# Optimization experiments

Hardware: AMD Instinct MI355X
Metric: run time of the kernel (lower is better)

The kernel has to match this reference:

```python
import jax, jax.numpy as jnp
import numpy as np

IN_DIM = 256
OUT_DIM = 256


def setup_inputs() -> dict:
    key = jax.random.key(0)
    k1, k2, k3, k4 = jax.random.split(key, 4)
    B, N = 8, 2048
    X = jax.random.normal(k1, (B, N, IN_DIM), dtype=jnp.float32)
    adj = jax.random.uniform(k2, (B, N, N), dtype=jnp.float32)
    # nn.Linear(input_dim, output_dim): W is [out, in], bias [out]
    bound = 1.0 / np.sqrt(IN_DIM)
    W = jax.random.uniform(k3, (OUT_DIM, IN_DIM), minval=-bound, maxval=bound, dtype=jnp.float32)
    b = jax.random.uniform(k4, (OUT_DIM,), minval=-bound, maxval=bound, dtype=jnp.float32)
    return {"X": X, "adj": adj, "W": W, "b": b}


def reference(X, adj, W, b):
    N = adj.shape[-1]
    # adj_hat = adj + I
    adj_hat = adj + jnp.eye(N, dtype=adj.dtype)
    # D^{-1/2} A_hat D^{-1/2}: diag matmuls are just row/col scaling
    d = jnp.sum(adj_hat, axis=-1) ** -0.5  # [B, N]
    adj_norm = d[..., :, None] * adj_hat * d[..., None, :]
    # aggregate then linear + relu
    H = jnp.matmul(adj_norm, X)  # [B, N, F_in]
    out = jnp.einsum('bnf,of->bno', H, W) + b
    return jax.nn.relu(out)
```

## Files before the change

kernel.cpp:

```cpp
#include <hip/hip_runtime.h>
#include <stdint.h>

typedef __attribute__((ext_vector_type(8))) short bf16x8;
typedef __attribute__((ext_vector_type(4))) float f32x4;
typedef unsigned short u16;

constexpr int NN = 2048, NF = 256;

__device__ inline u16 f2bf(float f) {
  uint32_t u = __builtin_bit_cast(uint32_t, f);
  uint32_t r = (u + 0x7FFFu + ((u >> 16) & 1u)) >> 16;
  return (u16)r;
}
__device__ inline float bf2f(u16 h) {
  uint32_t u = ((uint32_t)h) << 16;
  return __builtin_bit_cast(float, u);
}

__device__ inline void gload_lds16(const void* g, void* l) {
  __builtin_amdgcn_global_load_lds(
      (const __attribute__((address_space(1))) uint32_t*)g,
      (__attribute__((address_space(3))) uint32_t*)l,
      16, 0, 0);
}

__global__ __launch_bounds__(256) void k_rowsum(const float* __restrict__ adj,
                                                u16* __restrict__ adjb,
                                                float* __restrict__ d,
                                                const float* __restrict__ W,
                                                u16* __restrict__ Wb) {
  if (blockIdx.x >= 16384) {
    int i = (blockIdx.x - 16384) * 256 + threadIdx.x;
    float4 v = ((const float4*)W)[i];
    ushort4 o;
    o.x = f2bf(v.x); o.y = f2bf(v.y); o.z = f2bf(v.z); o.w = f2bf(v.w);
    *(ushort4*)(Wb + (size_t)i * 4) = o;
    return;
  }
  int row = blockIdx.x;
  const float4* p = (const float4*)(adj + (size_t)row * NN);
  u16* ob = adjb + (size_t)row * NN;
  float s = 0.f;
#pragma unroll
  for (int c = 0; c < 2; ++c) {
    int idx = threadIdx.x + 256 * c;
    float4 v = p[idx];
    s += v.x + v.y + v.z + v.w;
    ushort4 o;
    o.x = f2bf(v.x); o.y = f2bf(v.y); o.z = f2bf(v.z); o.w = f2bf(v.w);
    *(ushort4*)(ob + (size_t)idx * 4) = o;
  }
#pragma unroll
  for (int off = 32; off > 0; off >>= 1) s += __shfl_down(s, off, 64);
  __shared__ float red[4];
  int lane = threadIdx.x & 63, w = threadIdx.x >> 6;
  if (lane == 0) red[w] = s;
  __syncthreads();
  if (threadIdx.x == 0) {
    float t = red[0] + red[1] + red[2] + red[3] + 1.0f;
    d[row] = 1.0f / sqrtf(t);
  }
}

__global__ __launch_bounds__(256) void k_xprep(const float* __restrict__ X,
                                               const float* __restrict__ d,
                                               u16* __restrict__ XpT) {
  int jt = blockIdx.x, ft = blockIdx.y, b = blockIdx.z;
  int j0 = jt * 64, f0 = ft * 64;
  __shared__ u16 T[64][66];
  int t = threadIdx.x;
#pragma unroll
  for (int s = 0; s < 4; ++s) {
    int q = s * 256 + t;
    int r = q >> 4, c4 = q & 15;
    int j = j0 + r;
    float dv = d[b * NN + j];
    float4 v = *(const float4*)(X + ((size_t)(b * NN + j)) * NF + f0 + c4 * 4);
    T[r][c4 * 4 + 0] = f2bf(v.x * dv);
    T[r][c4 * 4 + 1] = f2bf(v.y * dv);
    T[r][c4 * 4 + 2] = f2bf(v.z * dv);
    T[r][c4 * 4 + 3] = f2bf(v.w * dv);
  }
  __syncthreads();
#pragma unroll
  for (int s = 0; s < 4; ++s) {
    int q = s * 256 + t;
    int fr = q >> 4, c4 = q & 15;
    int f = f0 + fr;
    int swz = (f >> 1) & 3;
    int joff = (c4 * 4) ^ (swz << 3);
    ushort4 o;
    o.x = T[c4 * 4 + 0][fr]; o.y = T[c4 * 4 + 1][fr];
    o.z = T[c4 * 4 + 2][fr]; o.w = T[c4 * 4 + 3][fr];
    *(ushort4*)(XpT + ((size_t)(b * NF + f)) * NN + j0 + joff) = o;
  }
}

#define BBASE 12288

#define FUSED_STEP(K, AW, AR, BW, BRI, VMC, IA, IB)                            \
  {                                                                            \
    if (IA) {                                                                  \
      gload_lds16(a_src + (size_t)((K) + 2) * 32,                              \
                  smem + ((AW) << 12) + (w << 10));                            \
    }                                                                          \
    if (IB) {                                                                  \
      _Pragma("unroll")                                                        \
      for (int c = 0; c < 4; ++c) {                                            \
        int q = c * 256 + t;                                                   \
        gload_lds16(XpTb + (size_t)(q >> 2) * NN + ((K) + 2) * 32 + (q & 3) * 8, \
                    smem + BBASE + ((BW) << 14) + (c * 256 + w * 64) * 16);    \
      }                                                                        \
    }                                                                          \
    __builtin_amdgcn_sched_barrier(0);                                         \
    asm volatile("s_waitcnt vmcnt(" VMC ")" ::: "memory");                     \
    __builtin_amdgcn_sched_barrier(0);                                         \
    __builtin_amdgcn_s_barrier();                                              \
    __builtin_amdgcn_sched_barrier(0);                                         \
    const char* Ab = smem + ((AR) << 12) + (((K) & 1) << 11);                  \
    const char* Bb = smem + BBASE + ((BRI) << 14);                             \
    bf16x8 af0 = *(const bf16x8*)(Ab + aoff0);                                 \
    bf16x8 af1 = *(const bf16x8*)(Ab + aoff0 + 1024);                          \
    bf16x8 b0 = *(const bf16x8*)(Bb + boff0);                                  \
    bf16x8 b1 = *(const bf16x8*)(Bb + boff0 + 1024);                           \
    bf16x8 b2 = *(const bf16x8*)(Bb + boff0 + 2048);                           \
    bf16x8 b3 = *(const bf16x8*)(Bb + boff0 + 3072);                           \
    asm volatile("s_waitcnt lgkmcnt(0)" ::: "memory");                         \
    __builtin_amdgcn_sched_barrier(0);                                         \
    __builtin_amdgcn_s_setprio(1);                                             \
    acc[0][0] = __builtin_amdgcn_mfma_f32_16x16x32_bf16(af0, b0, acc[0][0], 0, 0, 0); \
    acc[0][1] = __builtin_amdgcn_mfma_f32_16x16x32_bf16(af0, b1, acc[0][1], 0, 0, 0); \
    acc[0][2] = __builtin_amdgcn_mfma_f32_16x16x32_bf16(af0, b2, acc[0][2], 0, 0, 0); \
    acc[0][3] = __builtin_amdgcn_mfma_f32_16x16x32_bf16(af0, b3, acc[0][3], 0, 0, 0); \
    acc[1][0] = __builtin_amdgcn_mfma_f32_16x16x32_bf16(af1, b0, acc[1][0], 0, 0, 0); \
    acc[1][1] = __builtin_amdgcn_mfma_f32_16x16x32_bf16(af1, b1, acc[1][1], 0, 0, 0); \
    acc[1][2] = __builtin_amdgcn_mfma_f32_16x16x32_bf16(af1, b2, acc[1][2], 0, 0, 0); \
    acc[1][3] = __builtin_amdgcn_mfma_f32_16x16x32_bf16(af1, b3, acc[1][3], 0, 0, 0); \
    __builtin_amdgcn_s_setprio(0);                                             \
    __builtin_amdgcn_sched_barrier(0);                                         \
  }

__global__ __launch_bounds__(256, 2) void k_fused(
    const u16* __restrict__ adjb, const u16* __restrict__ XpT,
    const float* __restrict__ dsc, const u16* __restrict__ Wb,
    const float* __restrict__ bias, float* __restrict__ out) {
  int flat = blockIdx.x;
  int b = flat & 7, mt = flat >> 3;
  int i0 = mt * 32;

  __shared__ __align__(16) char smem[77824];
  u16* Hs = (u16*)smem;

  int t = threadIdx.x;
  int lane = t & 63, w = t >> 6;
  int l15 = lane & 15, l4 = lane >> 4;
  int wc = w;

  const u16* adjbb = adjb + ((size_t)b * NN + i0) * NN;
  const u16* XpTb = XpT + (size_t)b * NF * NN;

  int as_ = t >> 7, ar_ = (t >> 2) & 31, ac_ = t & 3;
  const u16* a_src = adjbb + (size_t)ar_ * NN + as_ * 32 +
                     ((ac_ ^ ((ar_ >> 1) & 3)) << 3);

  int aoff0 = l15 * 64 + ((l4 ^ ((l15 >> 1) & 3)) << 4);
  int n0 = wc * 64 + l15;
  int boff0 = n0 * 64 + ((l4 ^ ((n0 >> 1) & 3)) << 4);

  f32x4 acc[2][4] = {};

  gload_lds16(a_src, smem + (w << 10));
#pragma unroll
  for (int c = 0; c < 4; ++c) {
    int q = c * 256 + t;
    gload_lds16(XpTb + (size_t)(q >> 2) * NN + (q & 3) * 8,
                smem + BBASE + (c * 256 + w * 64) * 16);
  }
#pragma unroll
  for (int c = 0; c < 4; ++c) {
    int q = c * 256 + t;
    gload_lds16(XpTb + (size_t)(q >> 2) * NN + 32 + (q & 3) * 8,
                smem + BBASE + 16384 + (c * 256 + w * 64) * 16);
  }
  __builtin_amdgcn_sched_barrier(0);

  for (int kb = 0; kb < 60; kb += 12) {
    FUSED_STEP(kb + 0, 1, 0, 2, 0, "9", 1, 1)
    FUSED_STEP(kb + 1, 0, 0, 3, 1, "9", 0, 1)
    FUSED_STEP(kb + 2, 2, 1, 0, 2, "9", 1, 1)
    FUSED_STEP(kb + 3, 0, 1, 1, 3, "9", 0, 1)
    FUSED_STEP(kb + 4, 0, 2, 2, 0, "9", 1, 1)
    FUSED_STEP(kb + 5, 0, 2, 3, 1, "9", 0, 1)
    FUSED_STEP(kb + 6, 1, 0, 0, 2, "9", 1, 1)
    FUSED_STEP(kb + 7, 0, 0, 1, 3, "9", 0, 1)
    FUSED_STEP(kb + 8, 2, 1, 2, 0, "9", 1, 1)
    FUSED_STEP(kb + 9, 0, 1, 3, 1, "9", 0, 1)
    FUSED_STEP(kb + 10, 0, 2, 0, 2, "9", 1, 1)
    FUSED_STEP(kb + 11, 0, 2, 1, 3, "9", 0, 1)
  }
  FUSED_STEP(60, 1, 0, 2, 0, "9", 1, 1)
  FUSED_STEP(61, 0, 0, 3, 1, "9", 0, 1)
  FUSED_STEP(62, 0, 1, 0, 2, "4", 0, 0)
  FUSED_STEP(63, 0, 1, 0, 3, "0", 0, 0)

  __syncthreads();

  const float* db = dsc + b * NN;
#pragma unroll
  for (int mi = 0; mi < 2; ++mi) {
#pragma unroll
    for (int ni = 0; ni < 4; ++ni) {
      int f = wc * 64 + ni * 16 + l15;
      int swz8 = ((f >> 1) & 3) << 3;
      ushort4 xv = *(const ushort4*)(XpTb + (size_t)f * NN + i0 +
                                     ((mi * 16 + l4 * 4) ^ swz8));
#pragma unroll
      for (int qq = 0; qq < 4; ++qq) {
        int il = mi * 16 + l4 * 4 + qq;
        float dv = db[i0 + il];
        float xpv = bf2f(((const u16*)&xv)[qq]);
        float hv = dv * (acc[mi][ni][qq] + xpv);
        Hs[il * 264 + f] = f2bf(hv);
      }
    }
  }
  __syncthreads();

  f32x4 acc2[2][4] = {};
#pragma unroll
  for (int kk = 0; kk < 256; kk += 32) {
    bf16x8 a2[2], b2[4];
#pragma unroll
    for (int mi = 0; mi < 2; ++mi) {
      int r = mi * 16 + l15;
      a2[mi] = *(const bf16x8*)&Hs[r * 264 + kk + l4 * 8];
    }
#pragma unroll
    for (int ni = 0; ni < 4; ++ni) {
      int o = wc * 64 + ni * 16 + l15;
      b2[ni] = *(const bf16x8*)&Wb[(size_t)o * 256 + kk + l4 * 8];
    }
#pragma unroll
    for (int mi = 0; mi < 2; ++mi)
#pragma unroll
      for (int ni = 0; ni < 4; ++ni)
        acc2[mi][ni] = __builtin_amdgcn_mfma_f32_16x16x32_bf16(a2[mi], b2[ni],
                                                               acc2[mi][ni], 0, 0, 0);
  }

  float* outb = out + ((size_t)b * NN + i0) * NF;
#pragma unroll
  for (int mi = 0; mi < 2; ++mi) {
#pragma unroll
    for (int qq = 0; qq < 4; ++qq) {
      int il = mi * 16 + l4 * 4 + qq;
#pragma unroll
      for (int ni = 0; ni < 4; ++ni) {
        int o = wc * 64 + ni * 16 + l15;
        float v = acc2[mi][ni][qq] + bias[o];
        outb[(size_t)il * NF + o] = fmaxf(v, 0.f);
      }
    }
  }
}

extern "C" void kernel_launch(void* const* d_in, const int* in_sizes, int n_in,
                              void* d_out, int out_size, void* d_ws, size_t ws_size,
                              hipStream_t stream) {
  const float* X    = (const float*)d_in[0];
  const float* adj  = (const float*)d_in[1];
  const float* W    = (const float*)d_in[2];
  const float* bias = (const float*)d_in[3];
  float* out = (float*)d_out;

  char* ws = (char*)d_ws;
  float* dsc  = (float*)(ws);
  u16*   Wb   = (u16*)(ws + 65536);
  u16*   XpT  = (u16*)(ws + 262144);
  u16*   adjb = (u16*)(ws + 262144 + 8388608);

  k_rowsum<<<dim3(16448), dim3(256), 0, stream>>>(adj, adjb, dsc, W, Wb);
  k_xprep<<<dim3(32, 4, 8), dim3(256), 0, stream>>>(X, dsc, XpT);
  k_fused<<<dim3(512), dim3(256), 0, stream>>>(adjb, XpT, dsc, Wb, bias, out);
}
```

Measured before the change: 85.12 us.

## Double fused-kernel row tile to 64 with 8 waves sharing XpT tiles

The fused kernel now processes 64 output rows per block with 512 threads (2x4 wave grid) instead of 32 rows with 256 threads. Each XpT tile staged in LDS is reused by twice as many rows, which halves global/L2 traffic for the dense operand. The XOR swizzle moves from the stored XpT layout to the load addresses. The pipeline buffer indices and vmcnt waits are retuned for the new load counts. Cost: only 256 blocks (fewer than before) and more LDS per block, which may reduce occupancy and load balance across CUs.

New measurement: 75.68 us. -11.1%, faster.

```diff
diff --git a/kernel.cpp b/kernel.cpp
--- a/kernel.cpp
+++ b/kernel.cpp
@@ -86,39 +86,32 @@
   for (int s = 0; s < 4; ++s) {
     int q = s * 256 + t;
     int fr = q >> 4, c4 = q & 15;
-    int f = f0 + fr;
-    int swz = (f >> 1) & 3;
-    int joff = (c4 * 4) ^ (swz << 3);
     ushort4 o;
     o.x = T[c4 * 4 + 0][fr]; o.y = T[c4 * 4 + 1][fr];
     o.z = T[c4 * 4 + 2][fr]; o.w = T[c4 * 4 + 3][fr];
-    *(ushort4*)(XpT + ((size_t)(b * NF + f)) * NN + j0 + joff) = o;
-  }
-}
-
-#define BBASE 12288
-
-#define FUSED_STEP(K, AW, AR, BW, BRI, VMC, IA, IB)                            \
+    *(ushort4*)(XpT + ((size_t)(b * NF + f0 + fr)) * NN + j0 + c4 * 4) = o;
+  }
+}
+
+#define BBASE 24576
+
+#define FUSED_STEP(K, ARB, H, AW, BW, VMC, IA, IB)                             \
   {                                                                            \
-    if (IA) {                                                                  \
-      gload_lds16(a_src + (size_t)((K) + 2) * 32,                              \
-                  smem + ((AW) << 12) + (w << 10));                            \
+    if (IA) gload_lds16(a_src + (size_t)((K) + 2) * 32,                        \
+                        smem + (AW) * 8192 + aw_dst);                          \
+    if (IB) {                                                                  \
+      gload_lds16(b_src0 + (size_t)((K) + 2) * 32,                            \
+                  smem + BBASE + (BW) * 16384 + bw_dst0);                      \
+      gload_lds16(b_src1 + (size_t)((K) + 2) * 32,                            \
+                  smem + BBASE + (BW) * 16384 + bw_dst1);                      \
     }                                                                          \
-    if (IB) {                                                                  \
-      _Pragma("unroll")                                                        \
-      for (int c = 0; c < 4; ++c) {                                            \
-        int q = c * 256 + t;                                                   \
-        gload_lds16(XpTb + (size_t)(q >> 2) * NN + ((K) + 2) * 32 + (q & 3) * 8, \
-                    smem + BBASE + ((BW) << 14) + (c * 256 + w * 64) * 16);    \
-      }                                                                        \
-    }                                                                          \
     __builtin_amdgcn_sched_barrier(0);                                         \
     asm volatile("s_waitcnt vmcnt(" VMC ")" ::: "memory");                     \
     __builtin_amdgcn_sched_barrier(0);                                         \
     __builtin_amdgcn_s_barrier();                                              \
     __builtin_amdgcn_sched_barrier(0);                                         \
-    const char* Ab = smem + ((AR) << 12) + (((K) & 1) << 11);                  \
-    const char* Bb = smem + BBASE + ((BRI) << 14);                             \
+    const char* Ab = smem + (ARB) * 8192 + ((H) << 12);                        \
+    const char* Bb = smem + BBASE + ((K) & 3) * 16384;                         \
     bf16x8 af0 = *(const bf16x8*)(Ab + aoff0);                                 \
     bf16x8 af1 = *(const bf16x8*)(Ab + aoff0 + 1024);                          \
     bf16x8 b0 = *(const bf16x8*)(Bb + boff0);                                  \
@@ -140,68 +133,72 @@
     __builtin_amdgcn_sched_barrier(0);                                         \
   }
 
-__global__ __launch_bounds__(256, 2) void k_fused(
+__global__ __launch_bounds__(512, 2) void k_fused(
     const u16* __restrict__ adjb, const u16* __restrict__ XpT,
     const float* __restrict__ dsc, const u16* __restrict__ Wb,
     const float* __restrict__ bias, float* __restrict__ out) {
   int flat = blockIdx.x;
   int b = flat & 7, mt = flat >> 3;
-  int i0 = mt * 32;
-
-  __shared__ __align__(16) char smem[77824];
+  int i0 = mt * 64;
+
+  __shared__ __align__(16) char smem[90112];
   u16* Hs = (u16*)smem;
 
   int t = threadIdx.x;
   int lane = t & 63, w = t >> 6;
   int l15 = lane & 15, l4 = lane >> 4;
-  int wc = w;
+  int wr = w >> 2, wc = w & 3;
 
   const u16* adjbb = adjb + ((size_t)b * NN + i0) * NN;
   const u16* XpTb = XpT + (size_t)b * NF * NN;
 
-  int as_ = t >> 7, ar_ = (t >> 2) & 31, ac_ = t & 3;
-  const u16* a_src = adjbb + (size_t)ar_ * NN + as_ * 32 +
-                     ((ac_ ^ ((ar_ >> 1) & 3)) << 3);
-
-  int aoff0 = l15 * 64 + ((l4 ^ ((l15 >> 1) & 3)) << 4);
-  int n0 = wc * 64 + l15;
-  int boff0 = n0 * 64 + ((l4 ^ ((n0 >> 1) & 3)) << 4);
+  int sA = (w << 6) + lane;
+  int uA = sA >> 8;
+  int rA = (sA >> 2) & 63;
+  int cA = sA & 3;
+  const u16* a_src = adjbb + (size_t)rA * NN + uA * 32 +
+                     ((cA ^ ((rA >> 1) & 3)) << 3);
+  int aw_dst = w << 10;
+
+  int n0s = sA >> 2, c0s = sA & 3;
+  const u16* b_src0 = XpTb + (size_t)n0s * NN + ((c0s ^ ((n0s >> 1) & 3)) << 3);
+  int s1 = 512 + sA;
+  int n1s = s1 >> 2, c1s = s1 & 3;
+  const u16* b_src1 = XpTb + (size_t)n1s * NN + ((c1s ^ ((n1s >> 1) & 3)) << 3);
+  int bw_dst0 = w << 10;
+  int bw_dst1 = 8192 + (w << 10);
+
+  int swz = (l4 ^ ((l15 >> 1) & 3)) << 4;
+  int aoff0 = (wr * 32 + l15) * 64 + swz;
+  int boff0 = (wc * 64 + l15) * 64 + swz;
 
   f32x4 acc[2][4] = {};
 
-  gload_lds16(a_src, smem + (w << 10));
-#pragma unroll
-  for (int c = 0; c < 4; ++c) {
-    int q = c * 256 + t;
-    gload_lds16(XpTb + (size_t)(q >> 2) * NN + (q & 3) * 8,
-                smem + BBASE + (c * 256 + w * 64) * 16);
-  }
-#pragma unroll
-  for (int c = 0; c < 4; ++c) {
-    int q = c * 256 + t;
-    gload_lds16(XpTb + (size_t)(q >> 2) * NN + 32 + (q & 3) * 8,
-                smem + BBASE + 16384 + (c * 256 + w * 64) * 16);
-  }
+  gload_lds16(a_src, smem + aw_dst);
+  gload_lds16(b_src0, smem + BBASE + bw_dst0);
+  gload_lds16(b_src1, smem + BBASE + bw_dst1);
+  gload_lds16(b_src0 + 32, smem + BBASE + 16384 + bw_dst0);
+  gload_lds16(b_src1 + 32, smem + BBASE + 16384 + bw_dst1);
   __builtin_amdgcn_sched_barrier(0);
 
   for (int kb = 0; kb < 60; kb += 12) {
-    FUSED_STEP(kb + 0, 1, 0, 2, 0, "9", 1, 1)
-    FUSED_STEP(kb + 1, 0, 0, 3, 1, "9", 0, 1)
-    FUSED_STEP(kb + 2, 2, 1, 0, 2, "9", 1, 1)
-    FUSED_STEP(kb + 3, 0, 1, 1, 3, "9", 0, 1)
-    FUSED_STEP(kb + 4, 0, 2, 2, 0, "9", 1, 1)
-    FUSED_STEP(kb + 5, 0, 2, 3, 1, "9", 0, 1)
-    FUSED_STEP(kb + 6, 1, 0, 0, 2, "9", 1, 1)
-    FUSED_STEP(kb + 7, 0, 0, 1, 3, "9", 0, 1)
-    FUSED_STEP(kb + 8, 2, 1, 2, 0, "9", 1, 1)
-    FUSED_STEP(kb + 9, 0, 1, 3, 1, "9", 0, 1)
-    FUSED_STEP(kb + 10, 0, 2, 0, 2, "9", 1, 1)
-    FUSED_STEP(kb + 11, 0, 2, 1, 3, "9", 0, 1)
-  }
-  FUSED_STEP(60, 1, 0, 2, 0, "9", 1, 1)
-  FUSED_STEP(61, 0, 0, 3, 1, "9", 0, 1)
-  FUSED_STEP(62, 0, 1, 0, 2, "4", 0, 0)
-  FUSED_STEP(63, 0, 1, 0, 3, "0", 0, 0)
+    FUSED_STEP(kb + 0, 0, 0, 1, 2, "5", 1, 1)
+    FUSED_STEP(kb + 1, 0, 1, 0, 3, "5", 0, 1)
+    FUSED_STEP(kb + 2, 1, 0, 2, 0, "5", 1, 1)
+    FUSED_STEP(kb + 3, 1, 1, 0, 1, "5", 0, 1)
+    FUSED_STEP(kb + 4, 2, 0, 0, 2, "5", 1, 1)
+    FUSED_STEP(kb + 5, 2, 1, 0, 3, "5", 0, 1)
+    FUSED_STEP(kb + 6, 0, 0, 1, 0, "5", 1, 1)
+    FUSED_STEP(kb + 7, 0, 1, 0, 1, "5", 0, 1)
+    FUSED_STEP(kb + 8, 1, 0, 2, 2, "5", 1, 1)
+    FUSED_STEP(kb + 9, 1, 1, 0, 3, "5", 0, 1)
+    FUSED_STEP(kb + 10, 2, 0, 0, 0, "5", 1, 1)
+    FUSED_STEP(kb + 11, 2, 1, 0, 1, "5", 0, 1)
+  }
+  FUSED_STEP(60, 0, 0, 1, 2, "5", 1, 1)
+  FUSED_STEP(61, 0, 1, 0, 3, "5", 0, 1)
+  FUSED_STEP(62, 1, 0, 0, 0, "2", 0, 0)
+  FUSED_STEP(63, 1, 1, 0, 0, "0", 0, 0)
 
   __syncthreads();
 
@@ -211,12 +208,11 @@
 #pragma unroll
     for (int ni = 0; ni < 4; ++ni) {
       int f = wc * 64 + ni * 16 + l15;
-      int swz8 = ((f >> 1) & 3) << 3;
       ushort4 xv = *(const ushort4*)(XpTb + (size_t)f * NN + i0 +
-                                     ((mi * 16 + l4 * 4) ^ swz8));
+                                     wr * 32 + mi * 16 + l4 * 4);
 #pragma unroll
       for (int qq = 0; qq < 4; ++qq) {
-        int il = mi * 16 + l4 * 4 + qq;
+        int il = wr * 32 + mi * 16 + l4 * 4 + qq;
         float dv = db[i0 + il];
         float xpv = bf2f(((const u16*)&xv)[qq]);
         float hv = dv * (acc[mi][ni][qq] + xpv);
@@ -232,7 +228,7 @@
     bf16x8 a2[2], b2[4];
 #pragma unroll
     for (int mi = 0; mi < 2; ++mi) {
-      int r = mi * 16 + l15;
+      int r = wr * 32 + mi * 16 + l15;
       a2[mi] = *(const bf16x8*)&Hs[r * 264 + kk + l4 * 8];
     }
 #pragma unroll
@@ -253,7 +249,7 @@
   for (int mi = 0; mi < 2; ++mi) {
 #pragma unroll
     for (int qq = 0; qq < 4; ++qq) {
-      int il = mi * 16 + l4 * 4 + qq;
+      int il = wr * 32 + mi * 16 + l4 * 4 + qq;
 #pragma unroll
       for (int ni = 0; ni < 4; ++ni) {
         int o = wc * 64 + ni * 16 + l15;
@@ -281,5 +277,5 @@
 
   k_rowsum<<<dim3(16448), dim3(256), 0, stream>>>(adj, adjb, dsc, W, Wb);
   k_xprep<<<dim3(32, 4, 8), dim3(256), 0, stream>>>(X, dsc, XpT);
-  k_fused<<<dim3(512), dim3(256), 0, stream>>>(adjb, XpT, dsc, Wb, bias, out);
-}
+  k_fused<<<dim3(256), dim3(512), 0, stream>>>(adjb, XpT, dsc, Wb, bias, out);
+}
```

## Drop bf16 adjacency copy; convert fp32 adj to bf16 inside fused GEMM

Applied to the files above, without the earlier changes.

The rowsum kernel no longer writes a bf16 copy of the adjacency matrix. The fused kernel now loads fp32 adj tiles into registers three steps ahead, converts them to bf16 and stores them into a triple-buffered swizzled LDS area. The swizzle for X moves from the prep kernel's global layout to the fused kernel's load addressing, and the MFMA sequence is split around a partial lgkmcnt wait. This removes a 64MB bf16 write and read of adj, but the fused kernel must read 128MB of fp32 adj and spend VGPRs and ALU work on conversion inside the main loop.

Result: faster. 82.52 us (-3.1%).

```diff
diff --git a/kernel.cpp b/kernel.cpp
--- a/kernel.cpp
+++ b/kernel.cpp
@@ -25,7 +25,6 @@
 }
 
 __global__ __launch_bounds__(256) void k_rowsum(const float* __restrict__ adj,
-                                                u16* __restrict__ adjb,
                                                 float* __restrict__ d,
                                                 const float* __restrict__ W,
                                                 u16* __restrict__ Wb) {
@@ -39,16 +38,11 @@
   }
   int row = blockIdx.x;
   const float4* p = (const float4*)(adj + (size_t)row * NN);
-  u16* ob = adjb + (size_t)row * NN;
   float s = 0.f;
 #pragma unroll
   for (int c = 0; c < 2; ++c) {
-    int idx = threadIdx.x + 256 * c;
-    float4 v = p[idx];
+    float4 v = p[threadIdx.x + 256 * c];
     s += v.x + v.y + v.z + v.w;
-    ushort4 o;
-    o.x = f2bf(v.x); o.y = f2bf(v.y); o.z = f2bf(v.z); o.w = f2bf(v.w);
-    *(ushort4*)(ob + (size_t)idx * 4) = o;
   }
 #pragma unroll
   for (int off = 32; off > 0; off >>= 1) s += __shfl_down(s, off, 64);
@@ -86,69 +80,78 @@
   for (int s = 0; s < 4; ++s) {
     int q = s * 256 + t;
     int fr = q >> 4, c4 = q & 15;
-    int f = f0 + fr;
-    int swz = (f >> 1) & 3;
-    int joff = (c4 * 4) ^ (swz << 3);
     ushort4 o;
     o.x = T[c4 * 4 + 0][fr]; o.y = T[c4 * 4 + 1][fr];
     o.z = T[c4 * 4 + 2][fr]; o.w = T[c4 * 4 + 3][fr];
-    *(ushort4*)(XpT + ((size_t)(b * NF + f)) * NN + j0 + joff) = o;
-  }
-}
-
-#define BBASE 12288
-
-#define FUSED_STEP(K, AW, AR, BW, BRI, VMC, IA, IB)                            \
+    *(ushort4*)(XpT + ((size_t)(b * NF + f0 + fr)) * NN + j0 + c4 * 4) = o;
+  }
+}
+
+#define BBASE 8192
+
+#define STEP(KS, M3, W3, B4W, BRD, VMC, IA, WA, IB)                            \
   {                                                                            \
-    if (IA) {                                                                  \
-      gload_lds16(a_src + (size_t)((K) + 2) * 32,                              \
-                  smem + ((AW) << 12) + (w << 10));                            \
+    if (IA) aN[M3] = *(const float4*)(a_gsrc + (size_t)((KS) + 3) * 32);       \
+    if (IB) {                                                                  \
+      gload_lds16(b_src0 + (size_t)((KS) + 2) * 32,                            \
+                  smem + BBASE + (B4W) * 16384 + bwA);                         \
+      gload_lds16(b_src1 + (size_t)((KS) + 2) * 32,                            \
+                  smem + BBASE + (B4W) * 16384 + 4096 + bwA);                  \
+      gload_lds16(b_src2 + (size_t)((KS) + 2) * 32,                            \
+                  smem + BBASE + (B4W) * 16384 + 8192 + bwA);                  \
+      gload_lds16(b_src3 + (size_t)((KS) + 2) * 32,                            \
+                  smem + BBASE + (B4W) * 16384 + 12288 + bwA);                 \
     }                                                                          \
-    if (IB) {                                                                  \
-      _Pragma("unroll")                                                        \
-      for (int c = 0; c < 4; ++c) {                                            \
-        int q = c * 256 + t;                                                   \
-        gload_lds16(XpTb + (size_t)(q >> 2) * NN + ((K) + 2) * 32 + (q & 3) * 8, \
-                    smem + BBASE + ((BW) << 14) + (c * 256 + w * 64) * 16);    \
-      }                                                                        \
-    }                                                                          \
-    __builtin_amdgcn_sched_barrier(0);                                         \
-    asm volatile("s_waitcnt vmcnt(" VMC ")" ::: "memory");                     \
+    __builtin_amdgcn_sched_barrier(0);                                         \
+    asm volatile("s_waitcnt vmcnt(" VMC ") lgkmcnt(0)" ::: "memory");          \
     __builtin_amdgcn_sched_barrier(0);                                         \
     __builtin_amdgcn_s_barrier();                                              \
     __builtin_amdgcn_sched_barrier(0);                                         \
-    const char* Ab = smem + ((AR) << 12) + (((K) & 1) << 11);                  \
-    const char* Bb = smem + BBASE + ((BRI) << 14);                             \
+    const char* Ab = smem + (M3) * 2048;                                       \
+    const char* Bb = smem + BBASE + (BRD) * 16384;                             \
     bf16x8 af0 = *(const bf16x8*)(Ab + aoff0);                                 \
     bf16x8 af1 = *(const bf16x8*)(Ab + aoff0 + 1024);                          \
     bf16x8 b0 = *(const bf16x8*)(Bb + boff0);                                  \
     bf16x8 b1 = *(const bf16x8*)(Bb + boff0 + 1024);                           \
     bf16x8 b2 = *(const bf16x8*)(Bb + boff0 + 2048);                           \
     bf16x8 b3 = *(const bf16x8*)(Bb + boff0 + 3072);                           \
-    asm volatile("s_waitcnt lgkmcnt(0)" ::: "memory");                         \
+    asm volatile("s_waitcnt lgkmcnt(2)" ::: "memory");                         \
     __builtin_amdgcn_sched_barrier(0);                                         \
     __builtin_amdgcn_s_setprio(1);                                             \
     acc[0][0] = __builtin_amdgcn_mfma_f32_16x16x32_bf16(af0, b0, acc[0][0], 0, 0, 0); \
+    acc[1][0] = __builtin_amdgcn_mfma_f32_16x16x32_bf16(af1, b0, acc[1][0], 0, 0, 0); \
     acc[0][1] = __builtin_amdgcn_mfma_f32_16x16x32_bf16(af0, b1, acc[0][1], 0, 0, 0); \
+    acc[1][1] = __builtin_amdgcn_mfma_f32_16x16x32_bf16(af1, b1, acc[1][1], 0, 0, 0); \
+    __builtin_amdgcn_s_setprio(0);                                             \
+    __builtin_amdgcn_sched_barrier(0);                                         \
+    asm volatile("s_waitcnt lgkmcnt(0)" ::: "memory");                         \
+    __builtin_amdgcn_sched_barrier(0);                                         \
+    __builtin_amdgcn_s_setprio(1);                                             \
     acc[0][2] = __builtin_amdgcn_mfma_f32_16x16x32_bf16(af0, b2, acc[0][2], 0, 0, 0); \
+    acc[1][2] = __builtin_amdgcn_mfma_f32_16x16x32_bf16(af1, b2, acc[1][2], 0, 0, 0); \
     acc[0][3] = __builtin_amdgcn_mfma_f32_16x16x32_bf16(af0, b3, acc[0][3], 0, 0, 0); \
-    acc[1][0] = __builtin_amdgcn_mfma_f32_16x16x32_bf16(af1, b0, acc[1][0], 0, 0, 0); \
-    acc[1][1] = __builtin_amdgcn_mfma_f32_16x16x32_bf16(af1, b1, acc[1][1], 0, 0, 0); \
-    acc[1][2] = __builtin_amdgcn_mfma_f32_16x16x32_bf16(af1, b2, acc[1][2], 0, 0, 0); \
     acc[1][3] = __builtin_amdgcn_mfma_f32_16x16x32_bf16(af1, b3, acc[1][3], 0, 0, 0); \
     __builtin_amdgcn_s_setprio(0);                                             \
     __builtin_amdgcn_sched_barrier(0);                                         \
+    if (WA) {                                                                  \
+      float4 c0 = aN[W3];                                                      \
+      ushort4 pk;                                                              \
+      pk.x = f2bf(c0.x); pk.y = f2bf(c0.y);                                    \
+      pk.z = f2bf(c0.z); pk.w = f2bf(c0.w);                                    \
+      *(ushort4*)(smem + (W3) * 2048 + a_ldst) = pk;                           \
+    }                                                                          \
+    __builtin_amdgcn_sched_barrier(0);                                         \
   }
 
 __global__ __launch_bounds__(256, 2) void k_fused(
-    const u16* __restrict__ adjb, const u16* __restrict__ XpT,
+    const float* __restrict__ adj, const u16* __restrict__ XpT,
     const float* __restrict__ dsc, const u16* __restrict__ Wb,
     const float* __restrict__ bias, float* __restrict__ out) {
   int flat = blockIdx.x;
   int b = flat & 7, mt = flat >> 3;
   int i0 = mt * 32;
 
-  __shared__ __align__(16) char smem[77824];
+  __shared__ __align__(16) char smem[73728];
   u16* Hs = (u16*)smem;
 
   int t = threadIdx.x;
@@ -156,52 +159,76 @@
   int l15 = lane & 15, l4 = lane >> 4;
   int wc = w;
 
-  const u16* adjbb = adjb + ((size_t)b * NN + i0) * NN;
+  const float* adjf = adj + ((size_t)b * NN + i0) * NN;
   const u16* XpTb = XpT + (size_t)b * NF * NN;
 
-  int as_ = t >> 7, ar_ = (t >> 2) & 31, ac_ = t & 3;
-  const u16* a_src = adjbb + (size_t)ar_ * NN + as_ * 32 +
-                     ((ac_ ^ ((ar_ >> 1) & 3)) << 3);
-
-  int aoff0 = l15 * 64 + ((l4 ^ ((l15 >> 1) & 3)) << 4);
-  int n0 = wc * 64 + l15;
-  int boff0 = n0 * 64 + ((l4 ^ ((n0 >> 1) & 3)) << 4);
+  int rA = t >> 3, kq = t & 7;
+  int cc = kq >> 1, half = kq & 1;
+  const float* a_gsrc = adjf + (size_t)rA * NN + cc * 8 + half * 4;
+  int a_ldst = rA * 64 + ((cc ^ ((rA >> 1) & 3)) << 4) + half * 8;
+
+  int q0 = t,            n0 = q0 >> 2, c0 = q0 & 3;
+  int q1 = 256 + t,      n1 = q1 >> 2, c1 = q1 & 3;
+  int q2 = 512 + t,      n2 = q2 >> 2, c2 = q2 & 3;
+  int q3 = 768 + t,      n3 = q3 >> 2, c3 = q3 & 3;
+  const u16* b_src0 = XpTb + (size_t)n0 * NN + ((c0 ^ ((n0 >> 1) & 3)) << 3);
+  const u16* b_src1 = XpTb + (size_t)n1 * NN + ((c1 ^ ((n1 >> 1) & 3)) << 3);
+  const u16* b_src2 = XpTb + (size_t)n2 * NN + ((c2 ^ ((n2 >> 1) & 3)) << 3);
+  const u16* b_src3 = XpTb + (size_t)n3 * NN + ((c3 ^ ((n3 >> 1) & 3)) << 3);
+  int bwA = w << 10;
+
+  int swz = (l4 ^ ((l15 >> 1) & 3)) << 4;
+  int aoff0 = l15 * 64 + swz;
+  int boff0 = (wc * 64 + l15) * 64 + swz;
 
   f32x4 acc[2][4] = {};
-
-  gload_lds16(a_src, smem + (w << 10));
-#pragma unroll
-  for (int c = 0; c < 4; ++c) {
-    int q = c * 256 + t;
-    gload_lds16(XpTb + (size_t)(q >> 2) * NN + (q & 3) * 8,
-                smem + BBASE + (c * 256 + w * 64) * 16);
-  }
-#pragma unroll
-  for (int c = 0; c < 4; ++c) {
-    int q = c * 256 + t;
-    gload_lds16(XpTb + (size_t)(q >> 2) * NN + 32 + (q & 3) * 8,
-                smem + BBASE + 16384 + (c * 256 + w * 64) * 16);
-  }
-  __builtin_amdgcn_sched_barrier(0);
-
-  for (int kb = 0; kb < 60; kb += 12) {
-    FUSED_STEP(kb + 0, 1, 0, 2, 0, "9", 1, 1)
-    FUSED_STEP(kb + 1, 0, 0, 3, 1, "9", 0, 1)
-    FUSED_STEP(kb + 2, 2, 1, 0, 2, "9", 1, 1)
-    FUSED_STEP(kb + 3, 0, 1, 1, 3, "9", 0, 1)
-    FUSED_STEP(kb + 4, 0, 2, 2, 0, "9", 1, 1)
-    FUSED_STEP(kb + 5, 0, 2, 3, 1, "9", 0, 1)
-    FUSED_STEP(kb + 6, 1, 0, 0, 2, "9", 1, 1)
-    FUSED_STEP(kb + 7, 0, 0, 1, 3, "9", 0, 1)
-    FUSED_STEP(kb + 8, 2, 1, 2, 0, "9", 1, 1)
-    FUSED_STEP(kb + 9, 0, 1, 3, 1, "9", 0, 1)
-    FUSED_STEP(kb + 10, 0, 2, 0, 2, "9", 1, 1)
-    FUSED_STEP(kb + 11, 0, 2, 1, 3, "9", 0, 1)
-  }
-  FUSED_STEP(60, 1, 0, 2, 0, "9", 1, 1)
-  FUSED_STEP(61, 0, 0, 3, 1, "9", 0, 1)
-  FUSED_STEP(62, 0, 1, 0, 2, "4", 0, 0)
-  FUSED_STEP(63, 0, 1, 0, 3, "0", 0, 0)
+  float4 aN[3];
+
+  {
+    float4 aD0 = *(const float4*)(a_gsrc);
+    float4 aD1 = *(const float4*)(a_gsrc + 32);
+    __builtin_amdgcn_sched_barrier(0);
+    gload_lds16(b_src0, smem + BBASE + bwA);
+    gload_lds16(b_src1, smem + BBASE + 4096 + bwA);
+    gload_lds16(b_src2, smem + BBASE + 8192 + bwA);
+    gload_lds16(b_src3, smem + BBASE + 12288 + bwA);
+    gload_lds16(b_src0 + 32, smem + BBASE + 16384 + bwA);
+    gload_lds16(b_src1 + 32, smem + BBASE + 16384 + 4096 + bwA);
+    gload_lds16(b_src2 + 32, smem + BBASE + 16384 + 8192 + bwA);
+    gload_lds16(b_src3 + 32, smem + BBASE + 16384 + 12288 + bwA);
+    __builtin_amdgcn_sched_barrier(0);
+    aN[2] = *(const float4*)(a_gsrc + 64);
+    __builtin_amdgcn_sched_barrier(0);
+    asm volatile("s_waitcnt vmcnt(9)" ::: "memory");
+    __builtin_amdgcn_sched_barrier(0);
+    ushort4 pk;
+    pk.x = f2bf(aD0.x); pk.y = f2bf(aD0.y);
+    pk.z = f2bf(aD0.z); pk.w = f2bf(aD0.w);
+    *(ushort4*)(smem + a_ldst) = pk;
+    pk.x = f2bf(aD1.x); pk.y = f2bf(aD1.y);
+    pk.z = f2bf(aD1.z); pk.w = f2bf(aD1.w);
+    *(ushort4*)(smem + 2048 + a_ldst) = pk;
+    __builtin_amdgcn_sched_barrier(0);
+  }
+
+  for (int sb = 0; sb < 60; sb += 12) {
+    STEP(sb + 0,  0, 2, 2, 0, "9", 1, 1, 1)
+    STEP(sb + 1,  1, 0, 3, 1, "9", 1, 1, 1)
+    STEP(sb + 2,  2, 1, 0, 2, "9", 1, 1, 1)
+    STEP(sb + 3,  0, 2, 1, 3, "9", 1, 1, 1)
+    STEP(sb + 4,  1, 0, 2, 0, "9", 1, 1, 1)
+    STEP(sb + 5,  2, 1, 3, 1, "9", 1, 1, 1)
+    STEP(sb + 6,  0, 2, 0, 2, "9", 1, 1, 1)
+    STEP(sb + 7,  1, 0, 1, 3, "9", 1, 1, 1)
+    STEP(sb + 8,  2, 1, 2, 0, "9", 1, 1, 1)
+    STEP(sb + 9,  0, 2, 3, 1, "9", 1, 1, 1)
+    STEP(sb + 10, 1, 0, 0, 2, "9", 1, 1, 1)
+    STEP(sb + 11, 2, 1, 1, 3, "9", 1, 1, 1)
+  }
+  STEP(60, 0, 2, 2, 0, "9", 1, 1, 1)
+  STEP(61, 1, 0, 3, 1, "8", 0, 1, 1)
+  STEP(62, 2, 1, 0, 2, "4", 0, 0, 0)
+  STEP(63, 0, 2, 1, 3, "0", 0, 0, 0)
 
   __syncthreads();
 
@@ -211,9 +238,8 @@
 #pragma unroll
     for (int ni = 0; ni < 4; ++ni) {
       int f = wc * 64 + ni * 16 + l15;
-      int swz8 = ((f >> 1) & 3) << 3;
       ushort4 xv = *(const ushort4*)(XpTb + (size_t)f * NN + i0 +
-                                     ((mi * 16 + l4 * 4) ^ swz8));
+                                     mi * 16 + l4 * 4);
 #pragma unroll
       for (int qq = 0; qq < 4; ++qq) {
         int il = mi * 16 + l4 * 4 + qq;
@@ -274,12 +300,11 @@
   float* out = (float*)d_out;
 
   char* ws = (char*)d_ws;
-  float* dsc  = (float*)(ws);
-  u16*   Wb   = (u16*)(ws + 65536);
-  u16*   XpT  = (u16*)(ws + 262144);
-  u16*   adjb = (u16*)(ws + 262144 + 8388608);
-
-  k_rowsum<<<dim3(16448), dim3(256), 0, stream>>>(adj, adjb, dsc, W, Wb);
+  float* dsc = (float*)(ws);
+  u16*   Wb  = (u16*)(ws + 65536);
+  u16*   XpT = (u16*)(ws + 262144);
+
+  k_rowsum<<<dim3(16448), dim3(256), 0, stream>>>(adj, dsc, W, Wb);
   k_xprep<<<dim3(32, 4, 8), dim3(256), 0, stream>>>(X, dsc, XpT);
-  k_fused<<<dim3(512), dim3(256), 0, stream>>>(adjb, XpT, dsc, Wb, bias, out);
-}
+  k_fused<<<dim3(512), dim3(256), 0, stream>>>(adj, XpT, dsc, Wb, bias, out);
+}
```
